# Kernel tuning notes

Measured on AMD Instinct MI355X. Metric: run time of the kernel, lower is better.

The kernel has to match this reference:

```python
import jax, jax.numpy as jnp
import numpy as np

EMBED = 512
HEADS = 8
HD = EMBED // HEADS


def setup_inputs() -> dict:
    key = jax.random.key(0)
    ks = jax.random.split(key, 8)
    N, L = 4, 2048
    queries = jax.random.normal(ks[0], (N, L, EMBED), dtype=jnp.float32)
    keys = jax.random.normal(ks[1], (N, L, EMBED), dtype=jnp.float32)
    values = jax.random.normal(ks[2], (N, L, EMBED), dtype=jnp.float32)
    s = 1.0 / np.sqrt(HD)
    Wq = jax.random.normal(ks[3], (HD, HD), dtype=jnp.float32) * s
    Wk = jax.random.normal(ks[4], (HD, HD), dtype=jnp.float32) * s
    Wv = jax.random.normal(ks[5], (HD, HD), dtype=jnp.float32) * s
    Wo = jax.random.normal(ks[6], (EMBED, EMBED), dtype=jnp.float32) * (1.0 / np.sqrt(EMBED))
    bo = jax.random.normal(ks[7], (EMBED,), dtype=jnp.float32) * 0.01
    return {"queries": queries, "keys": keys, "values": values,
            "Wq": Wq, "Wk": Wk, "Wv": Wv, "Wo": Wo, "bo": bo}


def reference(queries, keys, values, Wq, Wk, Wv, Wo, bo):
    N, Lq, _ = queries.shape
    Lk = keys.shape[1]
    # split heads: [N, L, H, D]
    q = queries.reshape(N, Lq, HEADS, HD)
    k = keys.reshape(N, Lk, HEADS, HD)
    v = values.reshape(N, Lk, HEADS, HD)
    # per-head linear projections (weights shared across heads); torch Linear: x @ W.T
    q = jnp.einsum('nqhd,ed->nqhe', q, Wq)
    k = jnp.einsum('nkhd,ed->nkhe', k, Wk)
    v = jnp.einsum('nkhd,ed->nkhe', v, Wv)
    # scores scaled by sqrt(embed_size) (as in the original, NOT sqrt(head_dim))
    energy = jnp.einsum('nqhd,nkhd->nhqk', q, k) / jnp.sqrt(jnp.float32(EMBED))
    attn = jax.nn.softmax(energy, axis=-1)
    out = jnp.einsum('nhqk,nkhd->nqhd', attn, v).reshape(N, Lq, EMBED)
    return out @ Wo.T + bo
```

## Files before the change

### kernel.cpp

```cpp
#include <hip/hip_runtime.h>
#include <math.h>

#define N_ 4
#define L_ 2048
#define E_ 512
#define H_ 8
#define D_ 64

#define QSCALE 0.06375871588055019f

typedef short s16x8 __attribute__((ext_vector_type(8)));
typedef float f32x4 __attribute__((ext_vector_type(4)));
typedef float f32x16 __attribute__((ext_vector_type(16)));
typedef unsigned int u32x4 __attribute__((ext_vector_type(4)));

typedef const __attribute__((address_space(1))) unsigned int ga_u32;
typedef __attribute__((address_space(3))) unsigned int lds_u32;

__device__ __forceinline__ void gl_lds16(const unsigned short* g, unsigned short* l) {
    __builtin_amdgcn_global_load_lds((ga_u32*)g, (lds_u32*)l, 16, 0, 0);
}
__device__ __forceinline__ float exp2a(float x) {
    float r; asm("v_exp_f32 %0, %1" : "=v"(r) : "v"(x)); return r;
}
__device__ __forceinline__ unsigned int cvtpk(float lo, float hi) {
    unsigned int r; asm("v_cvt_pk_bf16_f32 %0, %1, %2" : "=v"(r) : "v"(lo), "v"(hi)); return r;
}
__device__ __forceinline__ void swap32(unsigned int& a, unsigned int& b) {
    asm volatile("v_permlane32_swap_b32 %0, %1" : "+v"(a), "+v"(b));
}
__device__ __forceinline__ float max3f(float a, float b, float c) {
    return fmaxf(fmaxf(a, b), c);
}
__device__ __forceinline__ unsigned short f2bf(float x) {
    unsigned int u = __builtin_bit_cast(unsigned int, x);
    u = (u + 0x7FFFu + ((u >> 16) & 1u)) >> 16;
    return (unsigned short)u;
}
__device__ __forceinline__ float bflo(unsigned int w) {
    return __builtin_bit_cast(float, w << 16);
}
__device__ __forceinline__ float bfhi(unsigned int w) {
    return __builtin_bit_cast(float, w & 0xFFFF0000u);
}

__global__ __launch_bounds__(256) void wo_split_kernel(
    const float* __restrict__ Wo, unsigned short* __restrict__ Whi,
    unsigned short* __restrict__ Wlo)
{
    const int i = blockIdx.x * 256 + threadIdx.x;
    const float4 w = reinterpret_cast<const float4*>(Wo)[i];
    const unsigned int hxy = cvtpk(w.x, w.y);
    const unsigned int hzw = cvtpk(w.z, w.w);
    const unsigned int lxy = cvtpk(w.x - bflo(hxy), w.y - bfhi(hxy));
    const unsigned int lzw = cvtpk(w.z - bflo(hzw), w.w - bfhi(hzw));
    uint2 hh; hh.x = hxy; hh.y = hzw;
    uint2 ll; ll.x = lxy; ll.y = lzw;
    reinterpret_cast<uint2*>(Whi)[i] = hh;
    reinterpret_cast<uint2*>(Wlo)[i] = ll;
}

__global__ __launch_bounds__(256) void qkv_proj_kernel(
    const float* __restrict__ Q, const float* __restrict__ K, const float* __restrict__ V,
    const float* __restrict__ Wq, const float* __restrict__ Wk, const float* __restrict__ Wv,
    unsigned short* __restrict__ Qp, unsigned short* __restrict__ Kp,
    unsigned short* __restrict__ Vt)
{
    __shared__ __align__(16) unsigned short Xl[4096];
    __shared__ __align__(16) unsigned short Whl[4096];
    __shared__ __align__(16) unsigned short Wll[4096];
    __shared__ __align__(16) unsigned short Yl[64][72];

    const int tid = threadIdx.x;
    const int lt = blockIdx.x;
    const int nh = blockIdx.y;
    const int m  = blockIdx.z;
    const int n = nh >> 3, h = nh & 7;
    const int l0 = lt * 64;

    const float* __restrict__ in = (m == 0) ? Q : (m == 1) ? K : V;
    const float* __restrict__ W  = (m == 0) ? Wq : (m == 1) ? Wk : Wv;

    const int xr = tid >> 2;
    const int xc = (tid & 3) * 16;
    {
        const float* xs = in + (size_t)(n * L_ + l0 + xr) * E_ + h * D_ + xc;
        float4 a = reinterpret_cast<const float4*>(xs)[0];
        float4 b = reinterpret_cast<const float4*>(xs)[1];
        float4 c = reinterpret_cast<const float4*>(xs)[2];
        float4 d = reinterpret_cast<const float4*>(xs)[3];
        u32x4 w0, w1;
        w0[0] = cvtpk(a.x, a.y); w0[1] = cvtpk(a.z, a.w);
        w0[2] = cvtpk(b.x, b.y); w0[3] = cvtpk(b.z, b.w);
        w1[0] = cvtpk(c.x, c.y); w1[1] = cvtpk(c.z, c.w);
        w1[2] = cvtpk(d.x, d.y); w1[3] = cvtpk(d.z, d.w);
        const int base  = (xr * 64 + xc) ^ ((xr & 7) << 3);
        const int base2 = (xr * 64 + xc + 8) ^ ((xr & 7) << 3);
        *reinterpret_cast<u32x4*>(&Xl[base])  = w0;
        *reinterpret_cast<u32x4*>(&Xl[base2]) = w1;

        const float* wsrc = W + (size_t)xr * D_ + xc;
        float wv[16];
#pragma unroll
        for (int i = 0; i < 4; ++i) {
            const float4 t = reinterpret_cast<const float4*>(wsrc)[i];
            wv[i * 4 + 0] = t.x; wv[i * 4 + 1] = t.y;
            wv[i * 4 + 2] = t.z; wv[i * 4 + 3] = t.w;
        }
        if (m == 0) {
#pragma unroll
            for (int i = 0; i < 16; ++i) wv[i] *= QSCALE;
        }
        u32x4 hi0, hi1, lo0, lo1;
#pragma unroll
        for (int i = 0; i < 4; ++i) {
            const unsigned int hw = cvtpk(wv[2 * i], wv[2 * i + 1]);
            hi0[i] = hw;
            lo0[i] = cvtpk(wv[2 * i] - bflo(hw), wv[2 * i + 1] - bfhi(hw));
        }
#pragma unroll
        for (int i = 0; i < 4; ++i) {
            const unsigned int hw = cvtpk(wv[8 + 2 * i], wv[8 + 2 * i + 1]);
            hi1[i] = hw;
            lo1[i] = cvtpk(wv[8 + 2 * i] - bflo(hw), wv[8 + 2 * i + 1] - bfhi(hw));
        }
        *reinterpret_cast<u32x4*>(&Whl[base])  = hi0;
        *reinterpret_cast<u32x4*>(&Whl[base2]) = hi1;
        *reinterpret_cast<u32x4*>(&Wll[base])  = lo0;
        *reinterpret_cast<u32x4*>(&Wll[base2]) = lo1;
    }
    __syncthreads();

    const int wave = tid >> 6, lane = tid & 63;
    const int ql = lane & 15, g = lane >> 4;
    const int arow = wave * 16 + ql;

    f32x4 acc[4];
#pragma unroll
    for (int t = 0; t < 4; ++t) acc[t] = (f32x4){0.f, 0.f, 0.f, 0.f};

    if (m < 2) {
        s16x8 xf[2];
#pragma unroll
        for (int ks = 0; ks < 2; ++ks)
            xf[ks] = *reinterpret_cast<const s16x8*>(
                &Xl[(arow * 64 + ks * 32 + g * 8) ^ ((arow & 7) << 3)]);
#pragma unroll
        for (int t = 0; t < 4; ++t) {
            const int wrow = t * 16 + ql;
#pragma unroll
            for (int ks = 0; ks < 2; ++ks) {
                const s16x8 bh = *reinterpret_cast<const s16x8*>(
                    &Whl[(wrow * 64 + ks * 32 + g * 8) ^ ((wrow & 7) << 3)]);
                acc[t] = __builtin_amdgcn_mfma_f32_16x16x32_bf16(xf[ks], bh, acc[t], 0, 0, 0);
                const s16x8 bl = *reinterpret_cast<const s16x8*>(
                    &Wll[(wrow * 64 + ks * 32 + g * 8) ^ ((wrow & 7) << 3)]);
                acc[t] = __builtin_amdgcn_mfma_f32_16x16x32_bf16(xf[ks], bl, acc[t], 0, 0, 0);
            }
        }
    } else {
        s16x8 whf[2], wlf[2];
#pragma unroll
        for (int ks = 0; ks < 2; ++ks) {
            whf[ks] = *reinterpret_cast<const s16x8*>(
                &Whl[(arow * 64 + ks * 32 + g * 8) ^ ((arow & 7) << 3)]);
            wlf[ks] = *reinterpret_cast<const s16x8*>(
                &Wll[(arow * 64 + ks * 32 + g * 8) ^ ((arow & 7) << 3)]);
        }
#pragma unroll
        for (int t = 0; t < 4; ++t) {
            const int xrow = t * 16 + ql;
#pragma unroll
            for (int ks = 0; ks < 2; ++ks) {
                const s16x8 bx = *reinterpret_cast<const s16x8*>(
                    &Xl[(xrow * 64 + ks * 32 + g * 8) ^ ((xrow & 7) << 3)]);
                acc[t] = __builtin_amdgcn_mfma_f32_16x16x32_bf16(whf[ks], bx, acc[t], 0, 0, 0);
                acc[t] = __builtin_amdgcn_mfma_f32_16x16x32_bf16(wlf[ks], bx, acc[t], 0, 0, 0);
            }
        }
    }

#pragma unroll
    for (int t = 0; t < 4; ++t)
#pragma unroll
        for (int r = 0; r < 4; ++r)
            Yl[wave * 16 + g * 4 + r][t * 16 + ql] = f2bf(acc[t][r]);
    __syncthreads();

    const int orow = tid >> 2;
    const int oc = (tid & 3) * 16;
    const uint4 v0 = *reinterpret_cast<const uint4*>(&Yl[orow][oc]);
    const uint4 v1 = *reinterpret_cast<const uint4*>(&Yl[orow][oc + 8]);
    unsigned short* dst;
    if (m == 0)      dst = Qp + ((size_t)nh * L_ + l0 + orow) * D_ + oc;
    else if (m == 1) dst = Kp + ((size_t)nh * L_ + l0 + orow) * D_ + oc;
    else             dst = Vt + ((size_t)nh * D_ + orow) * L_ + l0 + oc;
    *reinterpret_cast<uint4*>(dst) = v0;
    *reinterpret_cast<uint4*>(dst + 8) = v1;
}

__global__ __launch_bounds__(512, 2) void attn_kernel(
    const unsigned short* __restrict__ Qp, const unsigned short* __restrict__ Kp,
    const unsigned short* __restrict__ Vt, unsigned short* __restrict__ AO)
{
    __shared__ __align__(16) unsigned short ST[2][5 * 4096];

    const int tid = threadIdx.x;
    const int phys = blockIdx.x;
    const int bid = (phys & 7) * 64 + (phys >> 3);
    const int qt = bid & 15;
    const int nh = bid >> 4;
    const int n = nh >> 3, h = nh & 7;
    const int q0 = qt * 128;
    const int wave = tid >> 6;
    const int half = wave >> 2;
    const int w4 = wave & 3;
    const int lane = tid & 63;
    const int l31 = lane & 31;
    const int hh  = lane >> 5;

    const unsigned short* __restrict__ Qb = Qp + (size_t)nh * (L_ * D_);
    const unsigned short* __restrict__ Kb = Kp + (size_t)nh * (L_ * D_);
    const unsigned short* __restrict__ Vb = Vt + (size_t)nh * (D_ * L_);

    unsigned short* const Kbuf0 = &ST[half][0];
    unsigned short* const Kbuf1 = &ST[half][4096];
    unsigned short* const Vbuf0 = &ST[half][2 * 4096];
    unsigned short* const Vbuf1 = &ST[half][3 * 4096];
    unsigned short* const Vbuf2 = &ST[half][4 * 4096];

    const int G0 = w4 * 64 + lane;
    const int G1 = G0 + 256;
    const int r0 = G0 >> 3, c0 = (G0 & 7) ^ (r0 & 7);
    const int r1 = G1 >> 3, c1 = (G1 & 7) ^ (r1 & 7);

    const int kbase = half * 1024;
    const unsigned short* ks0 = Kb + (size_t)(kbase + r0) * 64 + c0 * 8;
    const unsigned short* ks1 = Kb + (size_t)(kbase + r1) * 64 + c1 * 8;
    const unsigned short* vs0 = Vb + (size_t)r0 * L_ + kbase + c0 * 8;
    const unsigned short* vs1 = Vb + (size_t)r1 * L_ + kbase + c1 * 8;

    gl_lds16(ks0, Kbuf0 + w4 * 512);
    gl_lds16(ks1, Kbuf0 + 2048 + w4 * 512);
    gl_lds16(vs0, Vbuf0 + w4 * 512);
    gl_lds16(vs1, Vbuf0 + 2048 + w4 * 512);

    const int qrow = q0 + w4 * 32 + l31;
    s16x8 qfrag[4];
#pragma unroll
    for (int ks = 0; ks < 4; ++ks)
        qfrag[ks] = *reinterpret_cast<const s16x8*>(
            Qb + (size_t)qrow * D_ + ks * 16 + hh * 8);

    float m_ = -INFINITY;
    float lsum = 0.f;
    f32x16 ot[2];
    ot[0] = (f32x16)0.f;
    ot[1] = (f32x16)0.f;
    s16x8 pf[4];

    unsigned short* vprev = Vbuf2;
    unsigned short* vcur  = Vbuf0;
    unsigned short* vnext = Vbuf1;

    const int NT = (L_ / 2) / 64;

    for (int kt = 0; kt < NT; ++kt) {
        __syncthreads();
        if (kt + 1 < NT) {
            unsigned short* kn = ((kt + 1) & 1) ? Kbuf1 : Kbuf0;
            gl_lds16(ks0 + (kt + 1) * 4096, kn + w4 * 512);
            gl_lds16(ks1 + (kt + 1) * 4096, kn + 2048 + w4 * 512);
            gl_lds16(vs0 + (kt + 1) * 64,   vnext + w4 * 512);
            gl_lds16(vs1 + (kt + 1) * 64,   vnext + 2048 + w4 * 512);
        }
        const unsigned short* __restrict__ Kl = (kt & 1) ? Kbuf1 : Kbuf0;

        f32x16 st[2];
        __builtin_amdgcn_s_setprio(1);
#pragma unroll
        for (int kv = 0; kv < 2; ++kv) {
            st[kv] = (f32x16)0.f;
            const int krow = kv * 32 + l31;
#pragma unroll
            for (int ks = 0; ks < 4; ++ks) {
                const s16x8 kf = *reinterpret_cast<const s16x8*>(
                    &Kl[(krow * 64 + ks * 16 + hh * 8) ^ ((krow & 7) << 3)]);
                st[kv] = __builtin_amdgcn_mfma_f32_32x32x16_bf16(kf, qfrag[ks], st[kv], 0, 0, 0);
            }
        }

        if (kt) {
#pragma unroll
            for (int dt = 0; dt < 2; ++dt) {
                const int drow = dt * 32 + l31;
#pragma unroll
                for (int kc = 0; kc < 4; ++kc) {
                    const s16x8 vf = *reinterpret_cast<const s16x8*>(
                        &vprev[(drow * 64 + kc * 16 + hh * 8) ^ ((drow & 7) << 3)]);
                    ot[dt] = __builtin_amdgcn_mfma_f32_32x32x16_bf16(vf, pf[kc], ot[dt], 0, 0, 0);
                }
            }
        }
        __builtin_amdgcn_s_setprio(0);

        const float t0 = max3f(st[0][0],  st[0][1],  st[0][2]);
        const float t1 = max3f(st[0][3],  st[0][4],  st[0][5]);
        const float t2 = max3f(st[0][6],  st[0][7],  st[0][8]);
        const float t3 = max3f(st[0][9],  st[0][10], st[0][11]);
        const float t4 = max3f(st[0][12], st[0][13], st[0][14]);
        const float t5 = max3f(st[0][15], st[1][0],  st[1][1]);
        const float t6 = max3f(st[1][2],  st[1][3],  st[1][4]);
        const float t7 = max3f(st[1][5],  st[1][6],  st[1][7]);
        const float t8 = max3f(st[1][8],  st[1][9],  st[1][10]);
        const float t9 = max3f(st[1][11], st[1][12], st[1][13]);
        const float ta = fmaxf(st[1][14], st[1][15]);
        const float u0 = max3f(t0, t1, t2);
        const float u1 = max3f(t3, t4, t5);
        const float u2 = max3f(t6, t7, t8);
        const float u3 = fmaxf(t9, ta);
        float tmax = fmaxf(max3f(u0, u1, u2), u3);
        tmax = fmaxf(tmax, __shfl_xor(tmax, 32));

        if (!__all(tmax <= m_ + 8.f)) {
            const float newm = fmaxf(m_, tmax);
            const float corr = exp2a(m_ - newm);
            lsum *= corr;
            ot[0] *= corr;
            ot[1] *= corr;
            m_ = newm;
        }

#pragma unroll
        for (int kv = 0; kv < 2; ++kv)
#pragma unroll
            for (int i = 0; i < 16; ++i) st[kv][i] = exp2a(st[kv][i] - m_);

        {
            float s0 = 0.f, s1 = 0.f, s2 = 0.f, s3 = 0.f;
#pragma unroll
            for (int i = 0; i < 4; ++i) {
                s0 += st[0][i];      s1 += st[0][i + 4];
                s2 += st[0][i + 8];  s3 += st[0][i + 12];
                s0 += st[1][i];      s1 += st[1][i + 4];
                s2 += st[1][i + 8];  s3 += st[1][i + 12];
            }
            float ts = (s0 + s1) + (s2 + s3);
            ts += __shfl_xor(ts, 32);
            lsum += ts;
        }

#pragma unroll
        for (int kv = 0; kv < 2; ++kv) {
            unsigned int A0 = cvtpk(st[kv][0],  st[kv][1]),  B0 = cvtpk(st[kv][2],  st[kv][3]);
            unsigned int A1 = cvtpk(st[kv][4],  st[kv][5]),  B1 = cvtpk(st[kv][6],  st[kv][7]);
            unsigned int A2 = cvtpk(st[kv][8],  st[kv][9]),  B2 = cvtpk(st[kv][10], st[kv][11]);
            unsigned int A3 = cvtpk(st[kv][12], st[kv][13]), B3 = cvtpk(st[kv][14], st[kv][15]);
            swap32(A0, A1); swap32(B0, B1);
            swap32(A2, A3); swap32(B2, B3);
            u32x4 lo; lo[0] = A0; lo[1] = B0; lo[2] = A1; lo[3] = B1;
            u32x4 hi; hi[0] = A2; hi[1] = B2; hi[2] = A3; hi[3] = B3;
            pf[kv * 2 + 0] = __builtin_bit_cast(s16x8, lo);
            pf[kv * 2 + 1] = __builtin_bit_cast(s16x8, hi);
        }

        unsigned short* tmp = vprev;
        vprev = vcur; vcur = vnext; vnext = tmp;
    }

    __builtin_amdgcn_s_setprio(1);
#pragma unroll
    for (int dt = 0; dt < 2; ++dt) {
        const int drow = dt * 32 + l31;
#pragma unroll
        for (int kc = 0; kc < 4; ++kc) {
            const s16x8 vf = *reinterpret_cast<const s16x8*>(
                &vprev[(drow * 64 + kc * 16 + hh * 8) ^ ((drow & 7) << 3)]);
            ot[dt] = __builtin_amdgcn_mfma_f32_32x32x16_bf16(vf, pf[kc], ot[dt], 0, 0, 0);
        }
    }
    __builtin_amdgcn_s_setprio(0);

    __syncthreads();
    float* mrg = reinterpret_cast<float*>(&ST[1][0]);
    const int slot = ((w4 << 6) + lane) * 36;
    if (half == 1) {
        *reinterpret_cast<f32x16*>(&mrg[slot])      = ot[0];
        *reinterpret_cast<f32x16*>(&mrg[slot + 16]) = ot[1];
        mrg[slot + 32] = m_;
        mrg[slot + 33] = lsum;
    }
    __syncthreads();
    if (half == 0) {
        const f32x16 ob0 = *reinterpret_cast<const f32x16*>(&mrg[slot]);
        const f32x16 ob1 = *reinterpret_cast<const f32x16*>(&mrg[slot + 16]);
        const float mB = mrg[slot + 32];
        const float lB = mrg[slot + 33];
        const float mm = fmaxf(m_, mB);
        const float sA = exp2a(m_ - mm);
        const float sB = exp2a(mB - mm);
        const float inv = 1.f / (lsum * sA + lB * sB);
        ot[0] = ot[0] * sA + ob0 * sB;
        ot[1] = ot[1] * sA + ob1 * sB;

#pragma unroll
        for (int dt = 0; dt < 2; ++dt) {
#pragma unroll
            for (int r = 0; r < 4; ++r) {
                uint2 o;
                o.x = cvtpk(ot[dt][4 * r + 0] * inv, ot[dt][4 * r + 1] * inv);
                o.y = cvtpk(ot[dt][4 * r + 2] * inv, ot[dt][4 * r + 3] * inv);
                const size_t elem = ((size_t)n * L_ + qrow) * E_ + h * D_ + dt * 32 + r * 8 + hh * 4;
                *reinterpret_cast<uint2*>(AO + elem) = o;
            }
        }
    }
}

__global__ __launch_bounds__(256) void out_proj_kernel(
    const unsigned short* __restrict__ AO, const unsigned short* __restrict__ Whi,
    const unsigned short* __restrict__ Wlo, const float* __restrict__ bo,
    float* __restrict__ out)
{
    __shared__ __align__(16) unsigned short Adb[2][4096];
    __shared__ __align__(16) unsigned short Hdb[2][4096];
    __shared__ __align__(16) unsigned short Ldb[2][4096];

    const int tid = threadIdx.x;
    const int bid = blockIdx.x;
    const int mt = bid >> 3, nt = bid & 7;
    const int m0 = mt * 64, n0 = nt * 64;
    const int wave = tid >> 6, lane = tid & 63;
    const int ql = lane & 15, g = lane >> 4;

    const int G0 = wave * 64 + lane;
    const int G1 = G0 + 256;
    const int r0 = G0 >> 3, c0 = (G0 & 7) ^ (r0 & 7);
    const int r1 = G1 >> 3, c1 = (G1 & 7) ^ (r1 & 7);

    const unsigned short* as0 = AO + (size_t)(m0 + r0) * E_ + c0 * 8;
    const unsigned short* as1 = AO + (size_t)(m0 + r1) * E_ + c1 * 8;
    const unsigned short* hs0 = Whi + (size_t)(n0 + r0) * E_ + c0 * 8;
    const unsigned short* hs1 = Whi + (size_t)(n0 + r1) * E_ + c1 * 8;
    const unsigned short* ls0 = Wlo + (size_t)(n0 + r0) * E_ + c0 * 8;
    const unsigned short* ls1 = Wlo + (size_t)(n0 + r1) * E_ + c1 * 8;

    gl_lds16(as0, &Adb[0][wave * 512]);
    gl_lds16(as1, &Adb[0][2048 + wave * 512]);
    gl_lds16(hs0, &Hdb[0][wave * 512]);
    gl_lds16(hs1, &Hdb[0][2048 + wave * 512]);
    gl_lds16(ls0, &Ldb[0][wave * 512]);
    gl_lds16(ls1, &Ldb[0][2048 + wave * 512]);

    float bias[4];
#pragma unroll
    for (int t = 0; t < 4; ++t) bias[t] = bo[n0 + t * 16 + ql];

    f32x4 acc[4];
#pragma unroll
    for (int t = 0; t < 4; ++t) acc[t] = (f32x4){0.f, 0.f, 0.f, 0.f};

    const int arow = wave * 16 + ql;

    for (int kc = 0; kc < 8; ++kc) {
        const int b = kc & 1;
        __syncthreads();
        if (kc + 1 < 8) {
            const int nb = b ^ 1;
            const int ko = (kc + 1) * 64;
            gl_lds16(as0 + ko, &Adb[nb][wave * 512]);
            gl_lds16(as1 + ko, &Adb[nb][2048 + wave * 512]);
            gl_lds16(hs0 + ko, &Hdb[nb][wave * 512]);
            gl_lds16(hs1 + ko, &Hdb[nb][2048 + wave * 512]);
            gl_lds16(ls0 + ko, &Ldb[nb][wave * 512]);
            gl_lds16(ls1 + ko, &Ldb[nb][2048 + wave * 512]);
        }
        const unsigned short* __restrict__ Al = Adb[b];
        const unsigned short* __restrict__ Hl = Hdb[b];
        const unsigned short* __restrict__ Ll = Ldb[b];

        s16x8 af[2];
#pragma unroll
        for (int ks = 0; ks < 2; ++ks)
            af[ks] = *reinterpret_cast<const s16x8*>(
                &Al[(arow * 64 + ks * 32 + g * 8) ^ ((arow & 7) << 3)]);

        __builtin_amdgcn_s_setprio(1);
#pragma unroll
        for (int t = 0; t < 4; ++t) {
            const int wrow = t * 16 + ql;
#pragma unroll
            for (int ks = 0; ks < 2; ++ks) {
                const s16x8 bh = *reinterpret_cast<const s16x8*>(
                    &Hl[(wrow * 64 + ks * 32 + g * 8) ^ ((wrow & 7) << 3)]);
                acc[t] = __builtin_amdgcn_mfma_f32_16x16x32_bf16(af[ks], bh, acc[t], 0, 0, 0);
                const s16x8 bl = *reinterpret_cast<const s16x8*>(
                    &Ll[(wrow * 64 + ks * 32 + g * 8) ^ ((wrow & 7) << 3)]);
                acc[t] = __builtin_amdgcn_mfma_f32_16x16x32_bf16(af[ks], bl, acc[t], 0, 0, 0);
            }
        }
        __builtin_amdgcn_s_setprio(0);
    }

#pragma unroll
    for (int t = 0; t < 4; ++t) {
#pragma unroll
        for (int r = 0; r < 4; ++r) {
            out[(size_t)(m0 + wave * 16 + g * 4 + r) * E_ + n0 + t * 16 + ql] =
                acc[t][r] + bias[t];
        }
    }
}

extern "C" void kernel_launch(void* const* d_in, const int* in_sizes, int n_in,
                              void* d_out, int out_size, void* d_ws, size_t ws_size,
                              hipStream_t stream)
{
    const float* Q  = (const float*)d_in[0];
    const float* K  = (const float*)d_in[1];
    const float* V  = (const float*)d_in[2];
    const float* Wq = (const float*)d_in[3];
    const float* Wk = (const float*)d_in[4];
    const float* Wv = (const float*)d_in[5];
    const float* Wo = (const float*)d_in[6];
    const float* bo = (const float*)d_in[7];
    float* out = (float*)d_out;

    unsigned short* ws = (unsigned short*)d_ws;
    const size_t SZ = (size_t)N_ * H_ * L_ * D_;
    unsigned short* Qp  = ws;
    unsigned short* Kp  = ws + SZ;
    unsigned short* Vt  = ws + 2 * SZ;
    unsigned short* AO  = ws + 3 * SZ;
    unsigned short* Whi = ws + 4 * SZ;
    unsigned short* Wlo = ws + 4 * SZ + 262144;

    qkv_proj_kernel<<<dim3(32, 32, 3), 256, 0, stream>>>(Q, K, V, Wq, Wk, Wv, Qp, Kp, Vt);
    wo_split_kernel<<<256, 256, 0, stream>>>(Wo, Whi, Wlo);
    attn_kernel<<<512, 512, 0, stream>>>(Qp, Kp, Vt, AO);
    out_proj_kernel<<<(8192 / 64) * (E_ / 64), 256, 0, stream>>>(AO, Whi, Wlo, bo, out);
}
```

Baseline: 92.39 us.

## Load K and V fragments directly from global memory in attention kernel

The attention kernel no longer stages K and V tiles through LDS with async global-to-LDS copies and per-iteration block barriers. Each wave now reads its MFMA operand fragments straight from global memory (relying on L1/L2 caching), and LDS is used only for the final cross-half softmax merge. This removes the barrier and LDS traffic per key tile, but every wave re-fetches the same K/V data from cache and loses the prefetch overlap that hid load latency.

New measurement: 155.9 us. +68.7%, slower.

```diff
diff --git a/kernel.cpp b/kernel.cpp
--- a/kernel.cpp
+++ b/kernel.cpp
@@ -42,6 +42,9 @@
 }
 __device__ __forceinline__ float bfhi(unsigned int w) {
     return __builtin_bit_cast(float, w & 0xFFFF0000u);
+}
+__device__ __forceinline__ s16x8 ld8(const unsigned short* p) {
+    return *reinterpret_cast<const s16x8*>(p);
 }
 
 __global__ __launch_bounds__(256) void wo_split_kernel(
@@ -143,18 +146,15 @@
         s16x8 xf[2];
 #pragma unroll
         for (int ks = 0; ks < 2; ++ks)
-            xf[ks] = *reinterpret_cast<const s16x8*>(
-                &Xl[(arow * 64 + ks * 32 + g * 8) ^ ((arow & 7) << 3)]);
+            xf[ks] = ld8(&Xl[(arow * 64 + ks * 32 + g * 8) ^ ((arow & 7) << 3)]);
 #pragma unroll
         for (int t = 0; t < 4; ++t) {
             const int wrow = t * 16 + ql;
 #pragma unroll
             for (int ks = 0; ks < 2; ++ks) {
-                const s16x8 bh = *reinterpret_cast<const s16x8*>(
-                    &Whl[(wrow * 64 + ks * 32 + g * 8) ^ ((wrow & 7) << 3)]);
+                const s16x8 bh = ld8(&Whl[(wrow * 64 + ks * 32 + g * 8) ^ ((wrow & 7) << 3)]);
                 acc[t] = __builtin_amdgcn_mfma_f32_16x16x32_bf16(xf[ks], bh, acc[t], 0, 0, 0);
-                const s16x8 bl = *reinterpret_cast<const s16x8*>(
-                    &Wll[(wrow * 64 + ks * 32 + g * 8) ^ ((wrow & 7) << 3)]);
+                const s16x8 bl = ld8(&Wll[(wrow * 64 + ks * 32 + g * 8) ^ ((wrow & 7) << 3)]);
                 acc[t] = __builtin_amdgcn_mfma_f32_16x16x32_bf16(xf[ks], bl, acc[t], 0, 0, 0);
             }
         }
@@ -162,18 +162,15 @@
         s16x8 whf[2], wlf[2];
 #pragma unroll
         for (int ks = 0; ks < 2; ++ks) {
-            whf[ks] = *reinterpret_cast<const s16x8*>(
-                &Whl[(arow * 64 + ks * 32 + g * 8) ^ ((arow & 7) << 3)]);
-            wlf[ks] = *reinterpret_cast<const s16x8*>(
-                &Wll[(arow * 64 + ks * 32 + g * 8) ^ ((arow & 7) << 3)]);
+            whf[ks] = ld8(&Whl[(arow * 64 + ks * 32 + g * 8) ^ ((arow & 7) << 3)]);
+            wlf[ks] = ld8(&Wll[(arow * 64 + ks * 32 + g * 8) ^ ((arow & 7) << 3)]);
         }
 #pragma unroll
         for (int t = 0; t < 4; ++t) {
             const int xrow = t * 16 + ql;
 #pragma unroll
             for (int ks = 0; ks < 2; ++ks) {
-                const s16x8 bx = *reinterpret_cast<const s16x8*>(
-                    &Xl[(xrow * 64 + ks * 32 + g * 8) ^ ((xrow & 7) << 3)]);
+                const s16x8 bx = ld8(&Xl[(xrow * 64 + ks * 32 + g * 8) ^ ((xrow & 7) << 3)]);
                 acc[t] = __builtin_amdgcn_mfma_f32_16x16x32_bf16(whf[ks], bx, acc[t], 0, 0, 0);
                 acc[t] = __builtin_amdgcn_mfma_f32_16x16x32_bf16(wlf[ks], bx, acc[t], 0, 0, 0);
             }
@@ -203,7 +200,7 @@
     const unsigned short* __restrict__ Qp, const unsigned short* __restrict__ Kp,
     const unsigned short* __restrict__ Vt, unsigned short* __restrict__ AO)
 {
-    __shared__ __align__(16) unsigned short ST[2][5 * 4096];
+    __shared__ __align__(16) float MRG[9216];
 
     const int tid = threadIdx.x;
     const int phys = blockIdx.x;
@@ -223,34 +220,16 @@
     const unsigned short* __restrict__ Kb = Kp + (size_t)nh * (L_ * D_);
     const unsigned short* __restrict__ Vb = Vt + (size_t)nh * (D_ * L_);
 
-    unsigned short* const Kbuf0 = &ST[half][0];
-    unsigned short* const Kbuf1 = &ST[half][4096];
-    unsigned short* const Vbuf0 = &ST[half][2 * 4096];
-    unsigned short* const Vbuf1 = &ST[half][3 * 4096];
-    unsigned short* const Vbuf2 = &ST[half][4 * 4096];
-
-    const int G0 = w4 * 64 + lane;
-    const int G1 = G0 + 256;
-    const int r0 = G0 >> 3, c0 = (G0 & 7) ^ (r0 & 7);
-    const int r1 = G1 >> 3, c1 = (G1 & 7) ^ (r1 & 7);
-
     const int kbase = half * 1024;
-    const unsigned short* ks0 = Kb + (size_t)(kbase + r0) * 64 + c0 * 8;
-    const unsigned short* ks1 = Kb + (size_t)(kbase + r1) * 64 + c1 * 8;
-    const unsigned short* vs0 = Vb + (size_t)r0 * L_ + kbase + c0 * 8;
-    const unsigned short* vs1 = Vb + (size_t)r1 * L_ + kbase + c1 * 8;
-
-    gl_lds16(ks0, Kbuf0 + w4 * 512);
-    gl_lds16(ks1, Kbuf0 + 2048 + w4 * 512);
-    gl_lds16(vs0, Vbuf0 + w4 * 512);
-    gl_lds16(vs1, Vbuf0 + 2048 + w4 * 512);
+
+    const unsigned short* Kl31 = Kb + (size_t)(kbase + l31) * D_ + hh * 8;
+    const unsigned short* Vl31 = Vb + (size_t)l31 * L_ + kbase + hh * 8;
 
     const int qrow = q0 + w4 * 32 + l31;
     s16x8 qfrag[4];
 #pragma unroll
     for (int ks = 0; ks < 4; ++ks)
-        qfrag[ks] = *reinterpret_cast<const s16x8*>(
-            Qb + (size_t)qrow * D_ + ks * 16 + hh * 8);
+        qfrag[ks] = ld8(Qb + (size_t)qrow * D_ + ks * 16 + hh * 8);
 
     float m_ = -INFINITY;
     float lsum = 0.f;
@@ -259,33 +238,18 @@
     ot[1] = (f32x16)0.f;
     s16x8 pf[4];
 
-    unsigned short* vprev = Vbuf2;
-    unsigned short* vcur  = Vbuf0;
-    unsigned short* vnext = Vbuf1;
-
     const int NT = (L_ / 2) / 64;
 
     for (int kt = 0; kt < NT; ++kt) {
-        __syncthreads();
-        if (kt + 1 < NT) {
-            unsigned short* kn = ((kt + 1) & 1) ? Kbuf1 : Kbuf0;
-            gl_lds16(ks0 + (kt + 1) * 4096, kn + w4 * 512);
-            gl_lds16(ks1 + (kt + 1) * 4096, kn + 2048 + w4 * 512);
-            gl_lds16(vs0 + (kt + 1) * 64,   vnext + w4 * 512);
-            gl_lds16(vs1 + (kt + 1) * 64,   vnext + 2048 + w4 * 512);
-        }
-        const unsigned short* __restrict__ Kl = (kt & 1) ? Kbuf1 : Kbuf0;
-
         f32x16 st[2];
         __builtin_amdgcn_s_setprio(1);
 #pragma unroll
         for (int kv = 0; kv < 2; ++kv) {
             st[kv] = (f32x16)0.f;
-            const int krow = kv * 32 + l31;
+            const unsigned short* kp = Kl31 + (size_t)(kt * 64 + kv * 32) * D_;
 #pragma unroll
             for (int ks = 0; ks < 4; ++ks) {
-                const s16x8 kf = *reinterpret_cast<const s16x8*>(
-                    &Kl[(krow * 64 + ks * 16 + hh * 8) ^ ((krow & 7) << 3)]);
+                const s16x8 kf = ld8(kp + ks * 16);
                 st[kv] = __builtin_amdgcn_mfma_f32_32x32x16_bf16(kf, qfrag[ks], st[kv], 0, 0, 0);
             }
         }
@@ -293,11 +257,10 @@
         if (kt) {
 #pragma unroll
             for (int dt = 0; dt < 2; ++dt) {
-                const int drow = dt * 32 + l31;
+                const unsigned short* vp = Vl31 + (size_t)dt * 32 * L_ + (kt - 1) * 64;
 #pragma unroll
                 for (int kc = 0; kc < 4; ++kc) {
-                    const s16x8 vf = *reinterpret_cast<const s16x8*>(
-                        &vprev[(drow * 64 + kc * 16 + hh * 8) ^ ((drow & 7) << 3)]);
+                    const s16x8 vf = ld8(vp + kc * 16);
                     ot[dt] = __builtin_amdgcn_mfma_f32_32x32x16_bf16(vf, pf[kc], ot[dt], 0, 0, 0);
                 }
             }
@@ -363,39 +326,34 @@
             pf[kv * 2 + 0] = __builtin_bit_cast(s16x8, lo);
             pf[kv * 2 + 1] = __builtin_bit_cast(s16x8, hi);
         }
-
-        unsigned short* tmp = vprev;
-        vprev = vcur; vcur = vnext; vnext = tmp;
     }
 
     __builtin_amdgcn_s_setprio(1);
 #pragma unroll
     for (int dt = 0; dt < 2; ++dt) {
-        const int drow = dt * 32 + l31;
+        const unsigned short* vp = Vl31 + (size_t)dt * 32 * L_ + (NT - 1) * 64;
 #pragma unroll
         for (int kc = 0; kc < 4; ++kc) {
-            const s16x8 vf = *reinterpret_cast<const s16x8*>(
-                &vprev[(drow * 64 + kc * 16 + hh * 8) ^ ((drow & 7) << 3)]);
+            const s16x8 vf = ld8(vp + kc * 16);
             ot[dt] = __builtin_amdgcn_mfma_f32_32x32x16_bf16(vf, pf[kc], ot[dt], 0, 0, 0);
         }
     }
     __builtin_amdgcn_s_setprio(0);
 
     __syncthreads();
-    float* mrg = reinterpret_cast<float*>(&ST[1][0]);
     const int slot = ((w4 << 6) + lane) * 36;
     if (half == 1) {
-        *reinterpret_cast<f32x16*>(&mrg[slot])      = ot[0];
-        *reinterpret_cast<f32x16*>(&mrg[slot + 16]) = ot[1];
-        mrg[slot + 32] = m_;
-        mrg[slot + 33] = lsum;
+        *reinterpret_cast<f32x16*>(&MRG[slot])      = ot[0];
+        *reinterpret_cast<f32x16*>(&MRG[slot + 16]) = ot[1];
+        MRG[slot + 32] = m_;
+        MRG[slot + 33] = lsum;
     }
     __syncthreads();
     if (half == 0) {
-        const f32x16 ob0 = *reinterpret_cast<const f32x16*>(&mrg[slot]);
-        const f32x16 ob1 = *reinterpret_cast<const f32x16*>(&mrg[slot + 16]);
-        const float mB = mrg[slot + 32];
-        const float lB = mrg[slot + 33];
+        const f32x16 ob0 = *reinterpret_cast<const f32x16*>(&MRG[slot]);
+        const f32x16 ob1 = *reinterpret_cast<const f32x16*>(&MRG[slot + 16]);
+        const float mB = MRG[slot + 32];
+        const float lB = MRG[slot + 33];
         const float mm = fmaxf(m_, mB);
         const float sA = exp2a(m_ - mm);
         const float sB = exp2a(mB - mm);
@@ -482,8 +440,7 @@
         s16x8 af[2];
 #pragma unroll
         for (int ks = 0; ks < 2; ++ks)
-            af[ks] = *reinterpret_cast<const s16x8*>(
-                &Al[(arow * 64 + ks * 32 + g * 8) ^ ((arow & 7) << 3)]);
+            af[ks] = ld8(&Al[(arow * 64 + ks * 32 + g * 8) ^ ((arow & 7) << 3)]);
 
         __builtin_amdgcn_s_setprio(1);
 #pragma unroll
@@ -491,11 +448,9 @@
             const int wrow = t * 16 + ql;
 #pragma unroll
             for (int ks = 0; ks < 2; ++ks) {
-                const s16x8 bh = *reinterpret_cast<const s16x8*>(
-                    &Hl[(wrow * 64 + ks * 32 + g * 8) ^ ((wrow & 7) << 3)]);
+                const s16x8 bh = ld8(&Hl[(wrow * 64 + ks * 32 + g * 8) ^ ((wrow & 7) << 3)]);
                 acc[t] = __builtin_amdgcn_mfma_f32_16x16x32_bf16(af[ks], bh, acc[t], 0, 0, 0);
-                const s16x8 bl = *reinterpret_cast<const s16x8*>(
-                    &Ll[(wrow * 64 + ks * 32 + g * 8) ^ ((wrow & 7) << 3)]);
+                const s16x8 bl = ld8(&Ll[(wrow * 64 + ks * 32 + g * 8) ^ ((wrow & 7) << 3)]);
                 acc[t] = __builtin_amdgcn_mfma_f32_16x16x32_bf16(af[ks], bl, acc[t], 0, 0, 0);
             }
         }
```

## Double-buffer V tiles instead of triple-buffer, issuing V prefetch after a mid-loop barrier

Applied to the files above, without the earlier changes.

The attention kernel now keeps two V staging buffers instead of three. The next V tile is loaded into the buffer that was just consumed, after an added __syncthreads placed after the PV MFMAs. This cuts LDS per block (5→4 tiles per half) and reuses ST[0] for the merge scratch. The likely aim is lower LDS use to help occupancy, at the cost of a second barrier per iteration and less prefetch distance for V. Repeated LDS load casts are folded into an ld8 helper.

Result: slower. 94.49 us (+2.3%).

```diff
diff --git a/kernel.cpp b/kernel.cpp
--- a/kernel.cpp
+++ b/kernel.cpp
@@ -42,6 +42,9 @@
 }
 __device__ __forceinline__ float bfhi(unsigned int w) {
     return __builtin_bit_cast(float, w & 0xFFFF0000u);
+}
+__device__ __forceinline__ s16x8 ld8(const unsigned short* p) {
+    return *reinterpret_cast<const s16x8*>(p);
 }
 
 __global__ __launch_bounds__(256) void wo_split_kernel(
@@ -143,18 +146,15 @@
         s16x8 xf[2];
 #pragma unroll
         for (int ks = 0; ks < 2; ++ks)
-            xf[ks] = *reinterpret_cast<const s16x8*>(
-                &Xl[(arow * 64 + ks * 32 + g * 8) ^ ((arow & 7) << 3)]);
+            xf[ks] = ld8(&Xl[(arow * 64 + ks * 32 + g * 8) ^ ((arow & 7) << 3)]);
 #pragma unroll
         for (int t = 0; t < 4; ++t) {
             const int wrow = t * 16 + ql;
 #pragma unroll
             for (int ks = 0; ks < 2; ++ks) {
-                const s16x8 bh = *reinterpret_cast<const s16x8*>(
-                    &Whl[(wrow * 64 + ks * 32 + g * 8) ^ ((wrow & 7) << 3)]);
+                const s16x8 bh = ld8(&Whl[(wrow * 64 + ks * 32 + g * 8) ^ ((wrow & 7) << 3)]);
                 acc[t] = __builtin_amdgcn_mfma_f32_16x16x32_bf16(xf[ks], bh, acc[t], 0, 0, 0);
-                const s16x8 bl = *reinterpret_cast<const s16x8*>(
-                    &Wll[(wrow * 64 + ks * 32 + g * 8) ^ ((wrow & 7) << 3)]);
+                const s16x8 bl = ld8(&Wll[(wrow * 64 + ks * 32 + g * 8) ^ ((wrow & 7) << 3)]);
                 acc[t] = __builtin_amdgcn_mfma_f32_16x16x32_bf16(xf[ks], bl, acc[t], 0, 0, 0);
             }
         }
@@ -162,18 +162,15 @@
         s16x8 whf[2], wlf[2];
 #pragma unroll
         for (int ks = 0; ks < 2; ++ks) {
-            whf[ks] = *reinterpret_cast<const s16x8*>(
-                &Whl[(arow * 64 + ks * 32 + g * 8) ^ ((arow & 7) << 3)]);
-            wlf[ks] = *reinterpret_cast<const s16x8*>(
-                &Wll[(arow * 64 + ks * 32 + g * 8) ^ ((arow & 7) << 3)]);
+            whf[ks] = ld8(&Whl[(arow * 64 + ks * 32 + g * 8) ^ ((arow & 7) << 3)]);
+            wlf[ks] = ld8(&Wll[(arow * 64 + ks * 32 + g * 8) ^ ((arow & 7) << 3)]);
         }
 #pragma unroll
         for (int t = 0; t < 4; ++t) {
             const int xrow = t * 16 + ql;
 #pragma unroll
             for (int ks = 0; ks < 2; ++ks) {
-                const s16x8 bx = *reinterpret_cast<const s16x8*>(
-                    &Xl[(xrow * 64 + ks * 32 + g * 8) ^ ((xrow & 7) << 3)]);
+                const s16x8 bx = ld8(&Xl[(xrow * 64 + ks * 32 + g * 8) ^ ((xrow & 7) << 3)]);
                 acc[t] = __builtin_amdgcn_mfma_f32_16x16x32_bf16(whf[ks], bx, acc[t], 0, 0, 0);
                 acc[t] = __builtin_amdgcn_mfma_f32_16x16x32_bf16(wlf[ks], bx, acc[t], 0, 0, 0);
             }
@@ -203,7 +200,7 @@
     const unsigned short* __restrict__ Qp, const unsigned short* __restrict__ Kp,
     const unsigned short* __restrict__ Vt, unsigned short* __restrict__ AO)
 {
-    __shared__ __align__(16) unsigned short ST[2][5 * 4096];
+    __shared__ __align__(16) unsigned short ST[2][4 * 4096];
 
     const int tid = threadIdx.x;
     const int phys = blockIdx.x;
@@ -227,7 +224,6 @@
     unsigned short* const Kbuf1 = &ST[half][4096];
     unsigned short* const Vbuf0 = &ST[half][2 * 4096];
     unsigned short* const Vbuf1 = &ST[half][3 * 4096];
-    unsigned short* const Vbuf2 = &ST[half][4 * 4096];
 
     const int G0 = w4 * 64 + lane;
     const int G1 = G0 + 256;
@@ -249,8 +245,7 @@
     s16x8 qfrag[4];
 #pragma unroll
     for (int ks = 0; ks < 4; ++ks)
-        qfrag[ks] = *reinterpret_cast<const s16x8*>(
-            Qb + (size_t)qrow * D_ + ks * 16 + hh * 8);
+        qfrag[ks] = ld8(Qb + (size_t)qrow * D_ + ks * 16 + hh * 8);
 
     float m_ = -INFINITY;
     float lsum = 0.f;
@@ -259,10 +254,6 @@
     ot[1] = (f32x16)0.f;
     s16x8 pf[4];
 
-    unsigned short* vprev = Vbuf2;
-    unsigned short* vcur  = Vbuf0;
-    unsigned short* vnext = Vbuf1;
-
     const int NT = (L_ / 2) / 64;
 
     for (int kt = 0; kt < NT; ++kt) {
@@ -271,10 +262,9 @@
             unsigned short* kn = ((kt + 1) & 1) ? Kbuf1 : Kbuf0;
             gl_lds16(ks0 + (kt + 1) * 4096, kn + w4 * 512);
             gl_lds16(ks1 + (kt + 1) * 4096, kn + 2048 + w4 * 512);
-            gl_lds16(vs0 + (kt + 1) * 64,   vnext + w4 * 512);
-            gl_lds16(vs1 + (kt + 1) * 64,   vnext + 2048 + w4 * 512);
         }
         const unsigned short* __restrict__ Kl = (kt & 1) ? Kbuf1 : Kbuf0;
+        unsigned short* const vprev = (kt & 1) ? Vbuf0 : Vbuf1;
 
         f32x16 st[2];
         __builtin_amdgcn_s_setprio(1);
@@ -284,8 +274,7 @@
             const int krow = kv * 32 + l31;
 #pragma unroll
             for (int ks = 0; ks < 4; ++ks) {
-                const s16x8 kf = *reinterpret_cast<const s16x8*>(
-                    &Kl[(krow * 64 + ks * 16 + hh * 8) ^ ((krow & 7) << 3)]);
+                const s16x8 kf = ld8(&Kl[(krow * 64 + ks * 16 + hh * 8) ^ ((krow & 7) << 3)]);
                 st[kv] = __builtin_amdgcn_mfma_f32_32x32x16_bf16(kf, qfrag[ks], st[kv], 0, 0, 0);
             }
         }
@@ -296,13 +285,18 @@
                 const int drow = dt * 32 + l31;
 #pragma unroll
                 for (int kc = 0; kc < 4; ++kc) {
-                    const s16x8 vf = *reinterpret_cast<const s16x8*>(
-                        &vprev[(drow * 64 + kc * 16 + hh * 8) ^ ((drow & 7) << 3)]);
+                    const s16x8 vf = ld8(&vprev[(drow * 64 + kc * 16 + hh * 8) ^ ((drow & 7) << 3)]);
                     ot[dt] = __builtin_amdgcn_mfma_f32_32x32x16_bf16(vf, pf[kc], ot[dt], 0, 0, 0);
                 }
             }
         }
         __builtin_amdgcn_s_setprio(0);
+
+        __syncthreads();
+        if (kt + 1 < NT) {
+            gl_lds16(vs0 + (kt + 1) * 64, vprev + w4 * 512);
+            gl_lds16(vs1 + (kt + 1) * 64, vprev + 2048 + w4 * 512);
+        }
 
         const float t0 = max3f(st[0][0],  st[0][1],  st[0][2]);
         const float t1 = max3f(st[0][3],  st[0][4],  st[0][5]);
@@ -363,26 +357,23 @@
             pf[kv * 2 + 0] = __builtin_bit_cast(s16x8, lo);
             pf[kv * 2 + 1] = __builtin_bit_cast(s16x8, hi);
         }
-
-        unsigned short* tmp = vprev;
-        vprev = vcur; vcur = vnext; vnext = tmp;
-    }
-
+    }
+
+    unsigned short* const vlast = ((NT - 1) & 1) ? Vbuf1 : Vbuf0;
     __builtin_amdgcn_s_setprio(1);
 #pragma unroll
     for (int dt = 0; dt < 2; ++dt) {
         const int drow = dt * 32 + l31;
 #pragma unroll
         for (int kc = 0; kc < 4; ++kc) {
-            const s16x8 vf = *reinterpret_cast<const s16x8*>(
-                &vprev[(drow * 64 + kc * 16 + hh * 8) ^ ((drow & 7) << 3)]);
+            const s16x8 vf = ld8(&vlast[(drow * 64 + kc * 16 + hh * 8) ^ ((drow & 7) << 3)]);
             ot[dt] = __builtin_amdgcn_mfma_f32_32x32x16_bf16(vf, pf[kc], ot[dt], 0, 0, 0);
         }
     }
     __builtin_amdgcn_s_setprio(0);
 
     __syncthreads();
-    float* mrg = reinterpret_cast<float*>(&ST[1][0]);
+    float* mrg = reinterpret_cast<float*>(&ST[0][0]);
     const int slot = ((w4 << 6) + lane) * 36;
     if (half == 1) {
         *reinterpret_cast<f32x16*>(&mrg[slot])      = ot[0];
@@ -482,8 +473,7 @@
         s16x8 af[2];
 #pragma unroll
         for (int ks = 0; ks < 2; ++ks)
-            af[ks] = *reinterpret_cast<const s16x8*>(
-                &Al[(arow * 64 + ks * 32 + g * 8) ^ ((arow & 7) << 3)]);
+            af[ks] = ld8(&Al[(arow * 64 + ks * 32 + g * 8) ^ ((arow & 7) << 3)]);
 
         __builtin_amdgcn_s_setprio(1);
 #pragma unroll
@@ -491,11 +481,9 @@
             const int wrow = t * 16 + ql;
 #pragma unroll
             for (int ks = 0; ks < 2; ++ks) {
-                const s16x8 bh = *reinterpret_cast<const s16x8*>(
-                    &Hl[(wrow * 64 + ks * 32 + g * 8) ^ ((wrow & 7) << 3)]);
+                const s16x8 bh = ld8(&Hl[(wrow * 64 + ks * 32 + g * 8) ^ ((wrow & 7) << 3)]);
                 acc[t] = __builtin_amdgcn_mfma_f32_16x16x32_bf16(af[ks], bh, acc[t], 0, 0, 0);
-                const s16x8 bl = *reinterpret_cast<const s16x8*>(
-                    &Ll[(wrow * 64 + ks * 32 + g * 8) ^ ((wrow & 7) << 3)]);
+                const s16x8 bl = ld8(&Ll[(wrow * 64 + ks * 32 + g * 8) ^ ((wrow & 7) << 3)]);
                 acc[t] = __builtin_amdgcn_mfma_f32_16x16x32_bf16(af[ks], bl, acc[t], 0, 0, 0);
             }
         }
```
